# Kernel optimization log

Hardware: AMD Instinct MI355X
Metric: run time of the kernel (lower is better)

The kernel has to match this reference:

```python
import jax, jax.numpy as jnp
import numpy as np

N_FEAT = 9
D_MODEL = 128
N_HEADS = 4
LN_EPS = 1e-5


def setup_inputs() -> dict:
    key = jax.random.key(0)
    ks = jax.random.split(key, 16)
    d, F = D_MODEL, N_FEAT
    s = 0.02
    return {
        "x": jax.random.normal(ks[0], (8, 256, 16, F), dtype=jnp.float32),
        # per-band Linear(1, d): weight (F, d), bias (F, d)
        "band_W": jax.random.normal(ks[1], (F, d), dtype=jnp.float32) * s,
        "band_b": jax.random.normal(ks[2], (F, d), dtype=jnp.float32) * s,
        "freq_pos": jax.random.normal(ks[3], (1, F, d), dtype=jnp.float32) * s,
        # MultiheadAttention packed in-proj (3d, d) and out-proj (d, d)
        "in_proj_w": jax.random.normal(ks[4], (3 * d, d), dtype=jnp.float32) * s,
        "in_proj_b": jax.random.normal(ks[5], (3 * d,), dtype=jnp.float32) * s,
        "out_proj_w": jax.random.normal(ks[6], (d, d), dtype=jnp.float32) * s,
        "out_proj_b": jax.random.normal(ks[7], (d,), dtype=jnp.float32) * s,
        # gate: Linear(F*d, d)
        "gate_w": jax.random.normal(ks[8], (d, F * d), dtype=jnp.float32) * s,
        "gate_b": jax.random.normal(ks[9], (d,), dtype=jnp.float32) * s,
        # output_proj: Linear(F*d, 2d) -> GELU -> Linear(2d, d) -> LayerNorm(d)
        "proj1_w": jax.random.normal(ks[10], (2 * d, F * d), dtype=jnp.float32) * s,
        "proj1_b": jax.random.normal(ks[11], (2 * d,), dtype=jnp.float32) * s,
        "proj2_w": jax.random.normal(ks[12], (d, 2 * d), dtype=jnp.float32) * s,
        "proj2_b": jax.random.normal(ks[13], (d,), dtype=jnp.float32) * s,
        "ln_g": jnp.ones((d,), dtype=jnp.float32),
        "ln_b": jnp.zeros((d,), dtype=jnp.float32),
    }


def _forward(x, band_W, band_b, freq_pos, in_proj_w, in_proj_b,
             out_proj_w, out_proj_b, gate_w, gate_b,
             proj1_w, proj1_b, proj2_w, proj2_b, ln_g, ln_b):
    B, T, C, F = x.shape
    d, H = D_MODEL, N_HEADS
    dh = d // H
    N = B * T * C
    xf = x.reshape(N, F)
    # per-band Linear(1, d) + positional embedding -> (N, F, d)
    tok = xf[:, :, None] * band_W[None] + band_b[None] + freq_pos
    # packed QKV projection (torch MHA semantics)
    qkv = jnp.einsum('nfd,ed->nfe', tok, in_proj_w) + in_proj_b
    q, k, v = jnp.split(qkv, 3, axis=-1)
    q = q.reshape(N, F, H, dh)
    k = k.reshape(N, F, H, dh)
    v = v.reshape(N, F, H, dh)
    scores = jnp.einsum('nqhd,nkhd->nhqk', q, k) / jnp.sqrt(jnp.float32(dh))
    attn = jax.nn.softmax(scores, axis=-1)
    ctx = jnp.einsum('nhqk,nkhd->nqhd', attn, v).reshape(N, F, d)
    attn_out = ctx @ out_proj_w.T + out_proj_b
    flat = attn_out.reshape(N, F * d)
    gate = jax.nn.sigmoid(flat @ gate_w.T + gate_b)
    h = jax.nn.gelu(flat @ proj1_w.T + proj1_b, approximate=False)
    y = h @ proj2_w.T + proj2_b
    mu = jnp.mean(y, axis=-1, keepdims=True)
    var = jnp.mean(jnp.square(y - mu), axis=-1, keepdims=True)
    y = (y - mu) * jax.lax.rsqrt(var + LN_EPS) * ln_g + ln_b
    out = y * gate
    return out.reshape(B, T, C, d)


def reference(x, band_W, band_b, freq_pos, in_proj_w, in_proj_b,
              out_proj_w, out_proj_b, gate_w, gate_b,
              proj1_w, proj1_b, proj2_w, proj2_b, ln_g, ln_b):
    return _forward(x, band_W, band_b, freq_pos, in_proj_w, in_proj_b,
                    out_proj_w, out_proj_b, gate_w, gate_b,
                    proj1_w, proj1_b, proj2_w, proj2_b, ln_g, ln_b)
```

## Files before the change

kernel.cpp:

```cpp
#include <hip/hip_runtime.h>

namespace {
constexpr int FB = 9;
constexpr int FD = 1152;
constexpr float LN_EPS = 1e-5f;
constexpr int NT = 512;

typedef __attribute__((ext_vector_type(8))) short short8v;
typedef __attribute__((ext_vector_type(4))) float float4v;

constexpr int WSA_F  = 0;
constexpr int WSC_F  = 3456;
constexpr int COEF_F = 6912;
constexpr int BF_F   = 8352;
constexpr int OPA_F  = 8736;
constexpr int P2F_B  = 71808;
constexpr int WTA_B  = 137344;

constexpr int LDS_BYTES = 51200;
constexpr int L_GATE = 43008;
constexpr int L_COEF = 43008;
constexpr int L_SX   = 48768;
constexpr int L_LNP  = 16384;

constexpr int NB_WTA  = 72;
constexpr int NB_BIAS = 384;
constexpr int NB_P2   = 64;

__device__ __forceinline__ unsigned short f2bf(float f) {
    unsigned u = __builtin_bit_cast(unsigned, f);
    u += 0x7FFFu + ((u >> 16) & 1u);
    return (unsigned short)(u >> 16);
}
__device__ __forceinline__ unsigned pkr(float lo, float hi) {
    const unsigned a = __builtin_bit_cast(unsigned, lo) + 0x8000u;
    const unsigned b = __builtin_bit_cast(unsigned, hi) + 0x8000u;
    return __builtin_amdgcn_perm(b, a, 0x07060302u);
}
__device__ __forceinline__ float gelu_f(float v) {
    float z = 0.7978845608f * (v + 0.044715f * v * v * v);
    z = fminf(fmaxf(z, -15.f), 15.f);
    const float e = __expf(2.f * z);
    const float th = (e - 1.f) / (e + 1.f);
    return 0.5f * v * (1.f + th);
}
#define MFMA16x32(a, b, c) __builtin_amdgcn_mfma_f32_16x16x32_bf16(a, b, c, 0, 0, 0)
}

__global__ void precompAC(const float* __restrict__ bW, const float* __restrict__ bb,
                          const float* __restrict__ fp, const float* __restrict__ ipw,
                          const float* __restrict__ ipb, float* __restrict__ ws)
{
    __shared__ float sw[128], sc[128];
    const int f = blockIdx.x, t = threadIdx.x;
    if (t < 128) { sw[t] = bW[f * 128 + t]; sc[t] = bb[f * 128 + t] + fp[f * 128 + t]; }
    __syncthreads();
    const float* row = ipw + (size_t)t * 128;
    float a = 0.f, c = 0.f;
    for (int k = 0; k < 128; k += 4) {
        const float4 w = *(const float4*)(row + k);
        a += sw[k]*w.x + sw[k+1]*w.y + sw[k+2]*w.z + sw[k+3]*w.w;
        c += sc[k]*w.x + sc[k+1]*w.y + sc[k+2]*w.z + sc[k+3]*w.w;
    }
    ws[WSA_F + f * 384 + t] = a;
    ws[WSC_F + f * 384 + t] = c + ipb[t];
}

__global__ void precompScoreOPA(const float* __restrict__ ws, const float* __restrict__ opw,
                                float* __restrict__ wso)
{
    const int b = blockIdx.x, t = threadIdx.x;
    if (b == 0) {
        if (t >= 324) return;
        const int h = t / 81, r = t % 81, fq = r / 9, fk = r % 9;
        const float* A = ws + WSA_F;
        const float* C = ws + WSC_F;
        const float* aq = A + fq * 384 + h * 32;
        const float* ak = A + fk * 384 + 128 + h * 32;
        const float* cq = C + fq * 384 + h * 32;
        const float* ck = C + fk * 384 + 128 + h * 32;
        float s2 = 0.f, s1q = 0.f, s1k = 0.f, s0 = 0.f;
        #pragma unroll
        for (int d = 0; d < 32; ++d) {
            s2  += aq[d] * ak[d];
            s1q += aq[d] * ck[d];
            s1k += cq[d] * ak[d];
            s0  += cq[d] * ck[d];
        }
        const float sc = 0.17677669529663687f;
        float* row = wso + COEF_F + (h * 9 + fq) * 40;
        row[fk]      = s2  * sc;
        row[10 + fk] = s1q * sc;
        row[20 + fk] = s1k * sc;
        row[30 + fk] = s0  * sc;
    } else {
        const int id = (b - 1) * 512 + t;
        if (id >= 9216) return;
        const int row = id >> 7, j = id & 127;
        const int h = row / 18, kk = row - h * 18;
        const float* av = (kk < 9) ? (ws + WSA_F + kk * 384 + 256)
                                   : (ws + WSC_F + (kk - 9) * 384 + 256);
        const float* op = opw + (size_t)j * 128 + h * 32;
        const float* avh = av + h * 32;
        float s = 0.f;
        #pragma unroll
        for (int ii = 0; ii < 32; ++ii) s += op[ii] * avh[ii];
        wso[OPA_F + row * 128 + j] = s;
    }
}

__global__ __launch_bounds__(512)
void precompWBP(const float* __restrict__ gw, const float* __restrict__ gb,
                const float* __restrict__ p1w, const float* __restrict__ p1b,
                const float* __restrict__ opb, const float* __restrict__ p2w,
                const float* __restrict__ wsf,
                unsigned short* __restrict__ wta, unsigned short* __restrict__ p2f,
                float* __restrict__ ws)
{
    __shared__ float smem[128 * 73 + 128 * 49];
    const int bid = blockIdx.x, t = threadIdx.x;
    if (bid < NB_WTA) {
        float* s_opaT = smem;
        float* s_winT = smem + 128 * 73;
        const int fq = bid % 9, oct = bid / 9;
        const int e0 = oct * 48;
        for (int i = t; i < 9216; i += 512) {
            const int r = i >> 7, j = i & 127;
            s_opaT[j * 73 + r] = wsf[OPA_F + i];
        }
        for (int i = t; i < 6144; i += 512) {
            const int el = i >> 7, j = i & 127;
            const int e = e0 + el;
            const float* Win = (e < 128) ? gw + (size_t)e * FD : p1w + (size_t)(e - 128) * FD;
            s_winT[j * 49 + el] = Win[fq * 128 + j];
        }
        __syncthreads();
        for (int d = t; d < 3456; d += 512) {
            const int el = d / 72, r = d - el * 72;
            const int e = e0 + el;
            float acc = 0.f;
            #pragma unroll 8
            for (int j = 0; j < 128; ++j)
                acc += s_winT[j * 49 + el] * s_opaT[j * 73 + r];
            const int h = r / 18, kk = r - h * 18;
            const int K = (h * 9 + fq) * 18 + kk;
            const int ks = K >> 5, slot = K & 31;
            const int lane = (e & 15) + 16 * (slot >> 3);
            wta[((size_t)((e >> 4) * 21 + ks) * 64 + lane) * 8 + (slot & 7)] = f2bf(acc);
        }
        if (fq == 0) {
            for (int d = t; d < 48 * 24; d += 512) {
                const int el = d / 24, Kp = 648 + d % 24;
                const int e = e0 + el;
                const int ks = Kp >> 5, slot = Kp & 31;
                const int lane = (e & 15) + 16 * (slot >> 3);
                wta[((size_t)((e >> 4) * 21 + ks) * 64 + lane) * 8 + (slot & 7)] = 0;
            }
        }
    } else if (bid < NB_WTA + NB_BIAS) {
        const int e = bid - NB_WTA;
        const float* Win = (e < 128) ? gw + (size_t)e * FD : p1w + (size_t)(e - 128) * FD;
        float acc = 0.f;
        for (int m = t; m < FD; m += 512) acc += Win[m] * opb[m & 127];
        #pragma unroll
        for (int off = 32; off > 0; off >>= 1) acc += __shfl_xor(acc, off);
        const int lane = t & 63, wid = t >> 6;
        if (lane == 0) smem[wid] = acc;
        __syncthreads();
        if (t == 0) {
            float s = (e < 128) ? gb[e] : p1b[e - 128];
            #pragma unroll
            for (int w = 0; w < 8; ++w) s += smem[w];
            ws[BF_F + e] = s;
        }
    } else {
        const int id = (bid - NB_WTA - NB_BIAS) * 512 + t;
        const int j = id & 7, lane = (id >> 3) & 63, ks = (id >> 9) & 7, nt = id >> 12;
        const int i = nt * 16 + (lane & 15);
        const int r = ks * 32 + (lane >> 4) * 8 + j;
        p2f[id] = f2bf(p2w[i * 256 + r]);
    }
}

__global__ __launch_bounds__(NT, 4)
void fba_main(const float* __restrict__ x, const float* __restrict__ p2b,
              const float* __restrict__ lng, const float* __restrict__ lnb,
              const float* __restrict__ wsf,
              const unsigned short* __restrict__ p2frag,
              const unsigned short* __restrict__ wta,
              float* __restrict__ out)
{
    __shared__ float4 lds4[LDS_BYTES / 16];
    char* lds = (char*)lds4;
    unsigned short* hfrag = (unsigned short*)lds;
    float* lnp = (float*)(lds + L_LNP);
    unsigned short* gateb = (unsigned short*)(lds + L_GATE);
    float* scoef = (float*)(lds + L_COEF);
    float* sx    = (float*)(lds + L_SX);

    const int t = threadIdx.x, lane = t & 63, wid = t >> 6;
    const int col = lane & 15, rg = lane >> 4;
    const int n0 = blockIdx.x * 32;

    for (int i = t; i < 1440; i += NT) scoef[i] = wsf[COEF_F + i];
    for (int i = t; i < 288;  i += NT) sx[i] = x[(size_t)n0 * FB + i];
    if (t < 128) *(float4*)(lds + 40960 + t * 16) = float4{0.f, 0.f, 0.f, 0.f};
    __syncthreads();

    for (int id = t; id < 1152; id += NT) {
        const int p = id >> 5, g = id & 31;
        const int fq = p % 9;
        const float* cf = scoef + p * 40;
        const float* xg = sx + g * FB;
        const float xq = xg[fq];
        float sc[9];
        float m = -1e30f;
        #pragma unroll
        for (int fk = 0; fk < 9; ++fk) {
            const float xk = xg[fk];
            const float v = (cf[fk] * xk + cf[10 + fk]) * xq + cf[20 + fk] * xk + cf[30 + fk];
            sc[fk] = v;
            m = fmaxf(m, v);
        }
        float sum = 0.f;
        #pragma unroll
        for (int fk = 0; fk < 9; ++fk) { sc[fk] = __expf(sc[fk] - m); sum += sc[fk]; }
        const float inv = 1.f / sum;
        float v[18];
        #pragma unroll
        for (int fk = 0; fk < 9; ++fk) {
            const float a = sc[fk] * inv;
            v[fk]     = a * xg[fk];
            v[9 + fk] = a;
        }
        const int mg = g >> 4, gl = g & 15;
        const int K0 = p * 18;
        #pragma unroll
        for (int qq = 0; qq < 9; ++qq) {
            const int K = K0 + 2 * qq;
            const int ks = K >> 5, slot = K & 31;
            const int row = ks * 2 + mg;
            const int u = gl + 16 * (slot >> 3);
            *(unsigned*)(lds + row * 1024 + u * 16 + (slot & 7) * 2) = pkr(v[2 * qq], v[2 * qq + 1]);
        }
    }
    __syncthreads();

    const int ng = wid;
    float4v acc0[3], acc1[3];
    #pragma unroll
    for (int q = 0; q < 3; ++q) {
        const float b = wsf[BF_F + (ng * 3 + q) * 16 + col];
        acc0[q] = float4v{b, b, b, b};
        acc1[q] = float4v{b, b, b, b};
    }
    const unsigned short* bbase = wta + (size_t)(ng * 3) * 21 * 512 + lane * 8;
    #define BLOAD(ks, q) (*(const short8v*)(bbase + ((size_t)(q) * 21 + (ks)) * 512))
    short8v cur0 = BLOAD(0, 0), cur1 = BLOAD(0, 1), cur2 = BLOAD(0, 2);
    #pragma unroll 4
    for (int ks = 0; ks < 20; ++ks) {
        const short8v nxt0 = BLOAD(ks + 1, 0);
        const short8v nxt1 = BLOAD(ks + 1, 1);
        const short8v nxt2 = BLOAD(ks + 1, 2);
        const short8v a0 = *(const short8v*)(lds + ((ks * 2 + 0) * 64 + lane) * 16);
        const short8v a1 = *(const short8v*)(lds + ((ks * 2 + 1) * 64 + lane) * 16);
        acc0[0] = MFMA16x32(a0, cur0, acc0[0]);
        acc1[0] = MFMA16x32(a1, cur0, acc1[0]);
        acc0[1] = MFMA16x32(a0, cur1, acc0[1]);
        acc1[1] = MFMA16x32(a1, cur1, acc1[1]);
        acc0[2] = MFMA16x32(a0, cur2, acc0[2]);
        acc1[2] = MFMA16x32(a1, cur2, acc1[2]);
        cur0 = nxt0; cur1 = nxt1; cur2 = nxt2;
    }
    {
        const short8v a0 = *(const short8v*)(lds + ((20 * 2 + 0) * 64 + lane) * 16);
        const short8v a1 = *(const short8v*)(lds + ((20 * 2 + 1) * 64 + lane) * 16);
        acc0[0] = MFMA16x32(a0, cur0, acc0[0]);
        acc1[0] = MFMA16x32(a1, cur0, acc1[0]);
        acc0[1] = MFMA16x32(a0, cur1, acc0[1]);
        acc1[1] = MFMA16x32(a1, cur1, acc1[1]);
        acc0[2] = MFMA16x32(a0, cur2, acc0[2]);
        acc1[2] = MFMA16x32(a1, cur2, acc1[2]);
    }
    #undef BLOAD
    __syncthreads();

    #pragma unroll
    for (int q = 0; q < 3; ++q) {
        const int e = (ng * 3 + q) * 16 + col;
        #pragma unroll
        for (int j = 0; j < 4; ++j) {
            #pragma unroll
            for (int mi = 0; mi < 2; ++mi) {
                const float vv = (mi == 0) ? acc0[q][j] : acc1[q][j];
                const int token = mi * 16 + rg * 4 + j;
                if (e < 128) {
                    const float gv = 1.f / (1.f + __expf(-vv));
                    gateb[token * 128 + e] = (unsigned short)(gv * 65535.f + 0.5f);
                } else {
                    const int rr = e - 128;
                    const float hv = gelu_f(vv);
                    hfrag[mi * 4096 + (rr >> 5) * 512 + (rg * 4 + j + 16 * ((rr >> 3) & 3)) * 8 + (rr & 7)] = f2bf(hv);
                }
            }
        }
    }
    __syncthreads();

    {
        const int mm = wid & 1, nh = wid >> 1;
        float4v y[2];
        float lg[2], lb[2];
        #pragma unroll
        for (int nti = 0; nti < 2; ++nti) {
            const int i = (nh * 2 + nti) * 16 + col;
            const float b = p2b[i];
            y[nti] = float4v{b, b, b, b};
            lg[nti] = lng[i];
            lb[nti] = lnb[i];
        }
        #pragma unroll
        for (int ks = 0; ks < 8; ++ks) {
            const short8v ah = *(const short8v*)(hfrag + mm * 4096 + ks * 512 + lane * 8);
            #pragma unroll
            for (int nti = 0; nti < 2; ++nti) {
                const short8v bw = *(const short8v*)(p2frag + (((nh * 2 + nti) * 8 + ks) * 64 + lane) * 8);
                y[nti] = MFMA16x32(ah, bw, y[nti]);
            }
        }
        #pragma unroll
        for (int j = 0; j < 4; ++j) {
            const int token = mm * 16 + rg * 4 + j;
            float s = y[0][j] + y[1][j];
            float qq = y[0][j] * y[0][j] + y[1][j] * y[1][j];
            s  += __shfl_xor(s, 1);  s  += __shfl_xor(s, 2);
            s  += __shfl_xor(s, 4);  s  += __shfl_xor(s, 8);
            qq += __shfl_xor(qq, 1); qq += __shfl_xor(qq, 2);
            qq += __shfl_xor(qq, 4); qq += __shfl_xor(qq, 8);
            if (col == 0) {
                lnp[token * 8 + nh * 2]     = s;
                lnp[token * 8 + nh * 2 + 1] = qq;
            }
        }
        __syncthreads();
        #pragma unroll
        for (int j = 0; j < 4; ++j) {
            const int token = mm * 16 + rg * 4 + j;
            const float s  = lnp[token * 8] + lnp[token * 8 + 2] + lnp[token * 8 + 4] + lnp[token * 8 + 6];
            const float qq = lnp[token * 8 + 1] + lnp[token * 8 + 3] + lnp[token * 8 + 5] + lnp[token * 8 + 7];
            const float mu = s * (1.f / 128.f);
            const float var = qq * (1.f / 128.f) - mu * mu;
            const float inv = rsqrtf(var + LN_EPS);
            float* op = out + (size_t)(n0 + token) * 128;
            #pragma unroll
            for (int nti = 0; nti < 2; ++nti) {
                const int i = (nh * 2 + nti) * 16 + col;
                const float gv = (float)gateb[token * 128 + i] * (1.f / 65535.f);
                op[i] = ((y[nti][j] - mu) * inv * lg[nti] + lb[nti]) * gv;
            }
        }
    }
}

extern "C" void kernel_launch(void* const* d_in, const int* in_sizes, int n_in,
                              void* d_out, int out_size, void* d_ws, size_t ws_size,
                              hipStream_t stream)
{
    const float* x          = (const float*)d_in[0];
    const float* band_W     = (const float*)d_in[1];
    const float* band_b     = (const float*)d_in[2];
    const float* freq_pos   = (const float*)d_in[3];
    const float* in_proj_w  = (const float*)d_in[4];
    const float* in_proj_b  = (const float*)d_in[5];
    const float* out_proj_w = (const float*)d_in[6];
    const float* out_proj_b = (const float*)d_in[7];
    const float* gate_w     = (const float*)d_in[8];
    const float* gate_b     = (const float*)d_in[9];
    const float* proj1_w    = (const float*)d_in[10];
    const float* proj1_b    = (const float*)d_in[11];
    const float* proj2_w    = (const float*)d_in[12];
    const float* proj2_b    = (const float*)d_in[13];
    const float* ln_g       = (const float*)d_in[14];
    const float* ln_b       = (const float*)d_in[15];
    float* outp = (float*)d_out;

    float* wsf = (float*)d_ws;
    unsigned short* p2f = (unsigned short*)((char*)d_ws + P2F_B);
    unsigned short* wta = (unsigned short*)((char*)d_ws + WTA_B);

    const int Ntok = in_sizes[0] / FB;
    const int nblk = Ntok / 32;

    hipLaunchKernelGGL(precompAC,       dim3(9),   dim3(384), 0, stream, band_W, band_b, freq_pos, in_proj_w, in_proj_b, wsf);
    hipLaunchKernelGGL(precompScoreOPA, dim3(19),  dim3(512), 0, stream, wsf, out_proj_w, wsf);
    hipLaunchKernelGGL(precompWBP,      dim3(NB_WTA + NB_BIAS + NB_P2), dim3(512), 0, stream,
                       gate_w, gate_b, proj1_w, proj1_b, out_proj_b, proj2_w, wsf, wta, p2f, wsf);
    hipLaunchKernelGGL(fba_main,        dim3(nblk), dim3(NT), 0, stream,
                       x, proj2_b, ln_g, ln_b, wsf, p2f, wta, outp);
}
```

Baseline: 74.99 us.

## Merge weight precompute kernels from three launches into two

Folds the A/C projection, bias folding and proj2 fragment packing into one first kernel. The score-coefficient job and the out-proj x value product (OPA) move into a second kernel. Each WTA block now recomputes the OPA tile in shared memory from a transposed copy of out_proj_w, instead of reading it from a global workspace. This removes one kernel launch and a global round trip, but adds redundant OPA computation in every one of the 72 blocks and uses much more shared memory per block.

```diff
diff --git a/kernel.cpp b/kernel.cpp
--- a/kernel.cpp
+++ b/kernel.cpp
@@ -13,7 +13,6 @@
 constexpr int WSC_F  = 3456;
 constexpr int COEF_F = 6912;
 constexpr int BF_F   = 8352;
-constexpr int OPA_F  = 8736;
 constexpr int P2F_B  = 71808;
 constexpr int WTA_B  = 137344;
 
@@ -23,9 +22,10 @@
 constexpr int L_SX   = 48768;
 constexpr int L_LNP  = 16384;
 
-constexpr int NB_WTA  = 72;
+constexpr int NB_AC   = 9;
 constexpr int NB_BIAS = 384;
 constexpr int NB_P2   = 64;
+constexpr int NB_WTA  = 72;
 
 __device__ __forceinline__ unsigned short f2bf(float f) {
     unsigned u = __builtin_bit_cast(unsigned, f);
@@ -47,92 +47,99 @@
 #define MFMA16x32(a, b, c) __builtin_amdgcn_mfma_f32_16x16x32_bf16(a, b, c, 0, 0, 0)
 }
 
-__global__ void precompAC(const float* __restrict__ bW, const float* __restrict__ bb,
-                          const float* __restrict__ fp, const float* __restrict__ ipw,
-                          const float* __restrict__ ipb, float* __restrict__ ws)
+__global__ __launch_bounds__(512)
+void precompBase(const float* __restrict__ bW, const float* __restrict__ bb,
+                 const float* __restrict__ fp, const float* __restrict__ ipw,
+                 const float* __restrict__ ipb,
+                 const float* __restrict__ gw, const float* __restrict__ gb,
+                 const float* __restrict__ p1w, const float* __restrict__ p1b,
+                 const float* __restrict__ opb, const float* __restrict__ p2w,
+                 unsigned short* __restrict__ p2f, float* __restrict__ ws)
 {
-    __shared__ float sw[128], sc[128];
-    const int f = blockIdx.x, t = threadIdx.x;
-    if (t < 128) { sw[t] = bW[f * 128 + t]; sc[t] = bb[f * 128 + t] + fp[f * 128 + t]; }
-    __syncthreads();
-    const float* row = ipw + (size_t)t * 128;
-    float a = 0.f, c = 0.f;
-    for (int k = 0; k < 128; k += 4) {
-        const float4 w = *(const float4*)(row + k);
-        a += sw[k]*w.x + sw[k+1]*w.y + sw[k+2]*w.z + sw[k+3]*w.w;
-        c += sc[k]*w.x + sc[k+1]*w.y + sc[k+2]*w.z + sc[k+3]*w.w;
-    }
-    ws[WSA_F + f * 384 + t] = a;
-    ws[WSC_F + f * 384 + t] = c + ipb[t];
-}
-
-__global__ void precompScoreOPA(const float* __restrict__ ws, const float* __restrict__ opw,
-                                float* __restrict__ wso)
+    __shared__ float sbuf[264];
+    const int bid = blockIdx.x, t = threadIdx.x;
+    if (bid < NB_AC) {
+        const int f = bid;
+        if (t < 128) {
+            sbuf[t]       = bW[f * 128 + t];
+            sbuf[128 + t] = bb[f * 128 + t] + fp[f * 128 + t];
+        }
+        __syncthreads();
+        if (t < 384) {
+            const float* row = ipw + (size_t)t * 128;
+            float a = 0.f, c = 0.f;
+            for (int k = 0; k < 128; k += 4) {
+                const float4 w = *(const float4*)(row + k);
+                a += sbuf[k]*w.x + sbuf[k+1]*w.y + sbuf[k+2]*w.z + sbuf[k+3]*w.w;
+                c += sbuf[128+k]*w.x + sbuf[129+k]*w.y + sbuf[130+k]*w.z + sbuf[131+k]*w.w;
+            }
+            ws[WSA_F + f * 384 + t] = a;
+            ws[WSC_F + f * 384 + t] = c + ipb[t];
+        }
+    } else if (bid < NB_AC + NB_BIAS) {
+        const int e = bid - NB_AC;
+        const float* Win = (e < 128) ? gw + (size_t)e * FD : p1w + (size_t)(e - 128) * FD;
+        float acc = 0.f;
+        for (int m = t; m < FD; m += 512) acc += Win[m] * opb[m & 127];
+        #pragma unroll
+        for (int off = 32; off > 0; off >>= 1) acc += __shfl_xor(acc, off);
+        const int lane = t & 63, wid = t >> 6;
+        if (lane == 0) sbuf[256 + wid] = acc;
+        __syncthreads();
+        if (t == 0) {
+            float s = (e < 128) ? gb[e] : p1b[e - 128];
+            #pragma unroll
+            for (int w = 0; w < 8; ++w) s += sbuf[256 + w];
+            ws[BF_F + e] = s;
+        }
+    } else {
+        const int id = (bid - NB_AC - NB_BIAS) * 512 + t;
+        const int j = id & 7, lane = (id >> 3) & 63, ks = (id >> 9) & 7, nt = id >> 12;
+        const int i = nt * 16 + (lane & 15);
+        const int r = ks * 32 + (lane >> 4) * 8 + j;
+        p2f[id] = f2bf(p2w[i * 256 + r]);
+    }
+}
+
+__global__ __launch_bounds__(512)
+void precompWO(const float* __restrict__ gw, const float* __restrict__ p1w,
+               const float* __restrict__ opw, const float* __restrict__ wsf,
+               unsigned short* __restrict__ wta, float* __restrict__ ws)
 {
-    const int b = blockIdx.x, t = threadIdx.x;
-    if (b == 0) {
-        if (t >= 324) return;
-        const int h = t / 81, r = t % 81, fq = r / 9, fk = r % 9;
-        const float* A = ws + WSA_F;
-        const float* C = ws + WSC_F;
-        const float* aq = A + fq * 384 + h * 32;
-        const float* ak = A + fk * 384 + 128 + h * 32;
-        const float* cq = C + fq * 384 + h * 32;
-        const float* ck = C + fk * 384 + 128 + h * 32;
-        float s2 = 0.f, s1q = 0.f, s1k = 0.f, s0 = 0.f;
-        #pragma unroll
-        for (int d = 0; d < 32; ++d) {
-            s2  += aq[d] * ak[d];
-            s1q += aq[d] * ck[d];
-            s1k += cq[d] * ak[d];
-            s0  += cq[d] * ck[d];
-        }
-        const float sc = 0.17677669529663687f;
-        float* row = wso + COEF_F + (h * 9 + fq) * 40;
-        row[fk]      = s2  * sc;
-        row[10 + fk] = s1q * sc;
-        row[20 + fk] = s1k * sc;
-        row[30 + fk] = s0  * sc;
-    } else {
-        const int id = (b - 1) * 512 + t;
-        if (id >= 9216) return;
-        const int row = id >> 7, j = id & 127;
-        const int h = row / 18, kk = row - h * 18;
-        const float* av = (kk < 9) ? (ws + WSA_F + kk * 384 + 256)
-                                   : (ws + WSC_F + (kk - 9) * 384 + 256);
-        const float* op = opw + (size_t)j * 128 + h * 32;
-        const float* avh = av + h * 32;
-        float s = 0.f;
-        #pragma unroll
-        for (int ii = 0; ii < 32; ++ii) s += op[ii] * avh[ii];
-        wso[OPA_F + row * 128 + j] = s;
-    }
-}
-
-__global__ __launch_bounds__(512)
-void precompWBP(const float* __restrict__ gw, const float* __restrict__ gb,
-                const float* __restrict__ p1w, const float* __restrict__ p1b,
-                const float* __restrict__ opb, const float* __restrict__ p2w,
-                const float* __restrict__ wsf,
-                unsigned short* __restrict__ wta, unsigned short* __restrict__ p2f,
-                float* __restrict__ ws)
-{
-    __shared__ float smem[128 * 73 + 128 * 49];
+    __shared__ float smem[34432];
     const int bid = blockIdx.x, t = threadIdx.x;
     if (bid < NB_WTA) {
-        float* s_opaT = smem;
-        float* s_winT = smem + 128 * 73;
+        float* s_opwT = smem;
+        float* s_avcv = smem + 16512;
+        float* s_opaT = smem + 18816;
+        float* s_winT = smem + 28160;
         const int fq = bid % 9, oct = bid / 9;
         const int e0 = oct * 48;
-        for (int i = t; i < 9216; i += 512) {
-            const int r = i >> 7, j = i & 127;
-            s_opaT[j * 73 + r] = wsf[OPA_F + i];
-        }
-        for (int i = t; i < 6144; i += 512) {
-            const int el = i >> 7, j = i & 127;
+        for (int idx = t; idx < 16384; idx += 512) {
+            const int j = idx >> 7, i = idx & 127;
+            s_opwT[i * 129 + j] = opw[idx];
+        }
+        for (int idx = t; idx < 2304; idx += 512) {
+            const int kk = idx >> 7, i = idx & 127;
+            s_avcv[idx] = (kk < 9) ? wsf[WSA_F + kk * 384 + 256 + i]
+                                   : wsf[WSC_F + (kk - 9) * 384 + 256 + i];
+        }
+        for (int idx = t; idx < 6144; idx += 512) {
+            const int el = idx >> 7, j = idx & 127;
             const int e = e0 + el;
             const float* Win = (e < 128) ? gw + (size_t)e * FD : p1w + (size_t)(e - 128) * FD;
             s_winT[j * 49 + el] = Win[fq * 128 + j];
+        }
+        __syncthreads();
+        for (int d = t; d < 9216; d += 512) {
+            const int r = d >> 7, j = d & 127;
+            const int h = r / 18, kk = r - h * 18;
+            const float* op = s_opwT + (h * 32) * 129 + j;
+            const float* av = s_avcv + kk * 128 + h * 32;
+            float acc = 0.f;
+            #pragma unroll 8
+            for (int ii = 0; ii < 32; ++ii) acc += op[ii * 129] * av[ii];
+            s_opaT[j * 73 + r] = acc;
         }
         __syncthreads();
         for (int d = t; d < 3456; d += 512) {
@@ -157,28 +164,29 @@
                 wta[((size_t)((e >> 4) * 21 + ks) * 64 + lane) * 8 + (slot & 7)] = 0;
             }
         }
-    } else if (bid < NB_WTA + NB_BIAS) {
-        const int e = bid - NB_WTA;
-        const float* Win = (e < 128) ? gw + (size_t)e * FD : p1w + (size_t)(e - 128) * FD;
-        float acc = 0.f;
-        for (int m = t; m < FD; m += 512) acc += Win[m] * opb[m & 127];
-        #pragma unroll
-        for (int off = 32; off > 0; off >>= 1) acc += __shfl_xor(acc, off);
-        const int lane = t & 63, wid = t >> 6;
-        if (lane == 0) smem[wid] = acc;
-        __syncthreads();
-        if (t == 0) {
-            float s = (e < 128) ? gb[e] : p1b[e - 128];
-            #pragma unroll
-            for (int w = 0; w < 8; ++w) s += smem[w];
-            ws[BF_F + e] = s;
-        }
     } else {
-        const int id = (bid - NB_WTA - NB_BIAS) * 512 + t;
-        const int j = id & 7, lane = (id >> 3) & 63, ks = (id >> 9) & 7, nt = id >> 12;
-        const int i = nt * 16 + (lane & 15);
-        const int r = ks * 32 + (lane >> 4) * 8 + j;
-        p2f[id] = f2bf(p2w[i * 256 + r]);
+        if (t >= 324) return;
+        const int h = t / 81, r = t % 81, fq = r / 9, fk = r % 9;
+        const float* A = wsf + WSA_F;
+        const float* C = wsf + WSC_F;
+        const float* aq = A + fq * 384 + h * 32;
+        const float* ak = A + fk * 384 + 128 + h * 32;
+        const float* cq = C + fq * 384 + h * 32;
+        const float* ck = C + fk * 384 + 128 + h * 32;
+        float s2 = 0.f, s1q = 0.f, s1k = 0.f, s0 = 0.f;
+        #pragma unroll
+        for (int d = 0; d < 32; ++d) {
+            s2  += aq[d] * ak[d];
+            s1q += aq[d] * ck[d];
+            s1k += cq[d] * ak[d];
+            s0  += cq[d] * ck[d];
+        }
+        const float sc = 0.17677669529663687f;
+        float* row = ws + COEF_F + (h * 9 + fq) * 40;
+        row[fk]      = s2  * sc;
+        row[10 + fk] = s1q * sc;
+        row[20 + fk] = s1k * sc;
+        row[30 + fk] = s0  * sc;
     }
 }
 
@@ -391,10 +399,11 @@
     const int Ntok = in_sizes[0] / FB;
     const int nblk = Ntok / 32;
 
-    hipLaunchKernelGGL(precompAC,       dim3(9),   dim3(384), 0, stream, band_W, band_b, freq_pos, in_proj_w, in_proj_b, wsf);
-    hipLaunchKernelGGL(precompScoreOPA, dim3(19),  dim3(512), 0, stream, wsf, out_proj_w, wsf);
-    hipLaunchKernelGGL(precompWBP,      dim3(NB_WTA + NB_BIAS + NB_P2), dim3(512), 0, stream,
-                       gate_w, gate_b, proj1_w, proj1_b, out_proj_b, proj2_w, wsf, wta, p2f, wsf);
-    hipLaunchKernelGGL(fba_main,        dim3(nblk), dim3(NT), 0, stream,
+    hipLaunchKernelGGL(precompBase, dim3(NB_AC + NB_BIAS + NB_P2), dim3(512), 0, stream,
+                       band_W, band_b, freq_pos, in_proj_w, in_proj_b,
+                       gate_w, gate_b, proj1_w, proj1_b, out_proj_b, proj2_w, p2f, wsf);
+    hipLaunchKernelGGL(precompWO, dim3(NB_WTA + 1), dim3(512), 0, stream,
+                       gate_w, proj1_w, out_proj_w, wsf, wta, wsf);
+    hipLaunchKernelGGL(fba_main,  dim3(nblk), dim3(NT), 0, stream,
                        x, proj2_b, ln_g, ln_b, wsf, p2f, wta, outp);
 }
```

Result: slower. 79.64 us (+6.2%).
